# Kernel optimization log

Hardware: AMD Instinct MI355X
Metric: run time of the kernel (lower is better)

Reference implementation:

```python
import jax, jax.numpy as jnp
import numpy as np

BS, C_IN, CTX, TGT = 2, 8, 1024, 96
D_MODEL, N_HEADS, D_FF, N_LAYERS = 256, 16, 1024, 4
PF, SF, PC, SC = 8, 4, 32, 16
NF = (CTX + SF - PF) // SF + 1   # 256 fine patches (incl. end-pad)
NC = (CTX + SC - PC) // SC + 1   # 64 coarse patches
TOTAL = NF + NC                  # 320
EPS = 1e-5
DK = D_MODEL // N_HEADS
SCALE = DK ** -0.5


def _patchify(z, plen, stride):
    # ReplicationPad1d((0, stride)) then unfold -> (bs, c, n_patches, plen)
    pad = jnp.broadcast_to(z[..., -1:], z.shape[:-1] + (stride,))
    zp = jnp.concatenate([z, pad], axis=-1)
    n = (zp.shape[-1] - plen) // stride + 1
    idx = np.arange(n)[:, None] * stride + np.arange(plen)[None, :]
    return zp[..., idx]


def _layernorm(x, s, b):
    m = x.mean(-1, keepdims=True)
    v = jnp.var(x, axis=-1, keepdims=True)
    return (x - m) * jax.lax.rsqrt(v + EPS) * s + b


def setup_inputs() -> dict:
    key = jax.random.key(0)
    ks = jax.random.split(key, 16)
    g = lambda k, shape: jax.random.normal(k, shape, jnp.float32) * 0.02
    return {
        "z": jax.random.normal(ks[0], (BS, C_IN, CTX), jnp.float32),
        "revin_w": jnp.ones((C_IN,), jnp.float32),
        "revin_b": jnp.zeros((C_IN,), jnp.float32),
        "Wf": g(ks[1], (PF, D_MODEL)), "bf": jnp.zeros((D_MODEL,), jnp.float32),
        "Wc": g(ks[2], (PC, D_MODEL)), "bc": jnp.zeros((D_MODEL,), jnp.float32),
        "W_pos": jax.random.uniform(ks[3], (TOTAL, D_MODEL), jnp.float32, -0.02, 0.02),
        "WQ": g(ks[4], (N_LAYERS, D_MODEL, D_MODEL)), "bQ": jnp.zeros((N_LAYERS, D_MODEL), jnp.float32),
        "WK": g(ks[5], (N_LAYERS, D_MODEL, D_MODEL)), "bK": jnp.zeros((N_LAYERS, D_MODEL), jnp.float32),
        "WV": g(ks[6], (N_LAYERS, D_MODEL, D_MODEL)), "bV": jnp.zeros((N_LAYERS, D_MODEL), jnp.float32),
        "WO": g(ks[7], (N_LAYERS, D_MODEL, D_MODEL)), "bO": jnp.zeros((N_LAYERS, D_MODEL), jnp.float32),
        "ln1_s": jnp.ones((N_LAYERS, D_MODEL), jnp.float32), "ln1_b": jnp.zeros((N_LAYERS, D_MODEL), jnp.float32),
        "ln2_s": jnp.ones((N_LAYERS, D_MODEL), jnp.float32), "ln2_b": jnp.zeros((N_LAYERS, D_MODEL), jnp.float32),
        "F1": g(ks[8], (N_LAYERS, D_MODEL, D_FF)), "c1": jnp.zeros((N_LAYERS, D_FF), jnp.float32),
        "F2": g(ks[9], (N_LAYERS, D_FF, D_MODEL)), "c2": jnp.zeros((N_LAYERS, D_MODEL), jnp.float32),
        "Wh": g(ks[10], (D_MODEL * TOTAL, TGT)), "bh": jnp.zeros((TGT,), jnp.float32),
    }


def reference(z, revin_w, revin_b, Wf, bf, Wc, bc, W_pos, WQ, bQ, WK, bK, WV, bV,
              WO, bO, ln1_s, ln1_b, ln2_s, ln2_b, F1, c1, F2, c2, Wh, bh):
    # RevIN norm over the time axis (last axis of (bs, c, T))
    mean = z.mean(-1, keepdims=True)
    std = jnp.sqrt(jnp.var(z, axis=-1, keepdims=True) + EPS)
    zn = (z - mean) / std * revin_w[None, :, None] + revin_b[None, :, None]

    # dual-scale patch embedding
    x_fine = _patchify(zn, PF, SF) @ Wf + bf      # (bs, c, NF, d)
    x_coarse = _patchify(zn, PC, SC) @ Wc + bc    # (bs, c, NC, d)
    x = jnp.concatenate([x_fine, x_coarse], axis=2)  # (bs, c, TOTAL, d)

    u = x.reshape(BS * C_IN, TOTAL, D_MODEL) + W_pos  # (B, S, d), B=bs*c

    # residual-score transformer encoder (post-norm)
    prev = None
    for l in range(N_LAYERS):
        q = (u @ WQ[l] + bQ[l]).reshape(-1, TOTAL, N_HEADS, DK).transpose(0, 2, 1, 3)
        k = (u @ WK[l] + bK[l]).reshape(-1, TOTAL, N_HEADS, DK).transpose(0, 2, 1, 3)
        v = (u @ WV[l] + bV[l]).reshape(-1, TOTAL, N_HEADS, DK).transpose(0, 2, 1, 3)
        s = jnp.einsum('bhqd,bhkd->bhqk', q, k) * SCALE
        if prev is not None:
            s = s + prev
        w = jax.nn.softmax(s, axis=-1)
        o = jnp.einsum('bhqk,bhkd->bhqd', w, v).transpose(0, 2, 1, 3).reshape(-1, TOTAL, D_MODEL)
        o = o @ WO[l] + bO[l]
        u = _layernorm(u + o, ln1_s[l], ln1_b[l])
        h = jax.nn.gelu(u @ F1[l] + c1[l], approximate=False) @ F2[l] + c2[l]
        u = _layernorm(u + h, ln2_s[l], ln2_b[l])
        prev = s

    # head: (bs, c, TOTAL, d) -> permute -> flatten(d, TOTAL) -> linear
    zz = u.reshape(BS, C_IN, TOTAL, D_MODEL).transpose(0, 1, 3, 2).reshape(BS, C_IN, D_MODEL * TOTAL)
    out = zz @ Wh + bh  # (bs, c, TGT)

    # RevIN denorm
    out = (out - revin_b[None, :, None]) / (revin_w[None, :, None] + EPS * EPS) * std + mean
    return out
```

## Files before the change

kernel.cpp:

```cpp
#include <hip/hip_runtime.h>
#include <math.h>

typedef unsigned short ushort;
typedef unsigned int uint;
typedef __attribute__((ext_vector_type(8))) short short8;
typedef __attribute__((ext_vector_type(4))) float f32x4;
typedef __attribute__((ext_vector_type(4))) ushort us4;

constexpr int BS = 2, C_IN = 8, CTX = 1024, TGT = 96;
constexpr int DM = 256, NH = 16, DFF = 1024, NL = 4;
constexpr int NF = 256, TOTAL = 320;
constexpr int NB = 16;
constexpr int DK = 16;
constexpr float EPS = 1e-5f;
constexpr float SCALE = 0.25f;
constexpr int KHEAD = DM * TOTAL;

__device__ __forceinline__ ushort f2b(float x) {
    uint u = __float_as_uint(x);
    u += 0x7fff + ((u >> 16) & 1);
    return (ushort)(u >> 16);
}
__device__ __forceinline__ float bu2f(ushort x) { return __uint_as_float(((uint)x) << 16); }
__device__ __forceinline__ float lo2f(uint p) { return __uint_as_float(p << 16); }
__device__ __forceinline__ float hi2f(uint p) { return __uint_as_float(p & 0xffff0000u); }
__device__ __forceinline__ uint pack2(float a, float b) { return (uint)f2b(a) | ((uint)f2b(b) << 16); }

__global__ void k_convt(const float* __restrict__ src, ushort* __restrict__ dst,
                        int R, int C, int sls, int dls) {
    __shared__ ushort tile[32][33];
    src += (size_t)blockIdx.z * sls;
    dst += (size_t)blockIdx.z * dls;
    int c0 = blockIdx.x * 32, r0 = blockIdx.y * 32;
    int tx = threadIdx.x, ty = threadIdx.y;
    tile[ty][tx] = f2b(src[(r0 + ty) * C + c0 + tx]);
    __syncthreads();
    dst[(c0 + ty) * R + r0 + tx] = tile[tx][ty];
}

__global__ void k_revin(const float* __restrict__ z, const float* __restrict__ rw,
                        const float* __restrict__ rb, float* __restrict__ zn,
                        float* __restrict__ meanv, float* __restrict__ stdv) {
    int bc = blockIdx.x, t = threadIdx.x;
    __shared__ float r1[256], r2[256];
    float s1 = 0.f, s2 = 0.f;
    for (int i = t; i < CTX; i += 256) {
        float x = z[bc * CTX + i];
        s1 += x; s2 += x * x;
    }
    r1[t] = s1; r2[t] = s2; __syncthreads();
    for (int off = 128; off > 0; off >>= 1) {
        if (t < off) { r1[t] += r1[t + off]; r2[t] += r2[t + off]; }
        __syncthreads();
    }
    float m = r1[0] * (1.0f / CTX);
    float var = r2[0] * (1.0f / CTX) - m * m;
    float sd = sqrtf(var + EPS);
    float w = rw[bc % C_IN], b = rb[bc % C_IN];
    float inv = 1.0f / sd;
    for (int i = t; i < CTX; i += 256) {
        float x = z[bc * CTX + i];
        zn[bc * CTX + i] = (x - m) * inv * w + b;
    }
    if (t == 0) { meanv[bc] = m; stdv[bc] = sd; }
}

__global__ void k_embed(const float* __restrict__ zn, const float* __restrict__ Wf,
                        const float* __restrict__ bfv, const float* __restrict__ Wc,
                        const float* __restrict__ bcv, const float* __restrict__ Wpos,
                        ushort* __restrict__ u) {
    int bc = blockIdx.x / TOTAL, p = blockIdx.x % TOTAL, d = threadIdx.x;
    float acc;
    if (p < NF) {
        acc = bfv[d];
        int base = p * 4;
        for (int i = 0; i < 8; i++) {
            int idx = min(base + i, CTX - 1);
            acc += zn[bc * CTX + idx] * Wf[i * DM + d];
        }
    } else {
        int pc = p - NF;
        acc = bcv[d];
        int base = pc * 16;
        for (int i = 0; i < 32; i++) {
            int idx = min(base + i, CTX - 1);
            acc += zn[bc * CTX + idx] * Wc[i * DM + d];
        }
    }
    acc += Wpos[p * DM + d];
    u[(bc * TOTAL + p) * DM + d] = f2b(acc);
}

template <int GELU, int QKV>
__global__ __launch_bounds__(256) void k_gemm_mfma(const ushort* __restrict__ A,
                                                   const ushort* __restrict__ Wt,
                                                   const float* __restrict__ b0,
                                                   const float* __restrict__ b1,
                                                   const float* __restrict__ b2,
                                                   ushort* __restrict__ C,
                                                   int M, int N, int K) {
    __shared__ ushort As[64][40];
    __shared__ ushort Bs[64][40];
    int tid = threadIdx.x;
    int wave = tid >> 6, lane = tid & 63;
    int quad = lane >> 4, l16 = lane & 15;
    int m0 = blockIdx.y * 64, n0 = blockIdx.x * 64;

    f32x4 acc[4];
#pragma unroll
    for (int nt = 0; nt < 4; nt++) acc[nt] = (f32x4){0.f, 0.f, 0.f, 0.f};

    int row = tid >> 2, kc = (tid & 3) * 8;
    for (int k0 = 0; k0 < K; k0 += 32) {
        *(short8*)&As[row][kc] = *(const short8*)&A[(m0 + row) * K + k0 + kc];
        *(short8*)&Bs[row][kc] = *(const short8*)&Wt[(n0 + row) * K + k0 + kc];
        __syncthreads();
        short8 af = *(const short8*)&As[wave * 16 + l16][quad * 8];
#pragma unroll
        for (int nt = 0; nt < 4; nt++) {
            short8 bf = *(const short8*)&Bs[nt * 16 + l16][quad * 8];
            acc[nt] = __builtin_amdgcn_mfma_f32_16x16x32_bf16(af, bf, acc[nt], 0, 0, 0);
        }
        __syncthreads();
    }
#pragma unroll
    for (int nt = 0; nt < 4; nt++) {
        int col = n0 + nt * 16 + l16;
        float bi;
        if (QKV) {
            int bs = (n0 + nt * 16) >> 8;
            const float* bp = bs == 0 ? b0 : (bs == 1 ? b1 : b2);
            bi = bp[col & 255];
        } else {
            bi = b0[col];
        }
#pragma unroll
        for (int r = 0; r < 4; r++) {
            int rowm = m0 + wave * 16 + quad * 4 + r;
            float vv = acc[nt][r] + bi;
            if (GELU) vv = vv * 0.5f * (1.0f + erff(vv * 0.70710678118f));
            if (QKV) C[(col >> 8) * (M * DM) + rowm * DM + (col & 255)] = f2b(vv);
            else C[rowm * N + col] = f2b(vv);
        }
    }
}

__global__ __launch_bounds__(256, 4) void k_attn(const ushort* __restrict__ qm, const ushort* __restrict__ km,
                                                 const ushort* __restrict__ vm, uint4* __restrict__ sp,
                                                 ushort* __restrict__ ao, int mode) {
    __shared__ ushort sh[10240];
    uint* sh32 = (uint*)sh;
    int bh = blockIdx.x, b = bh >> 4, h = bh & 15;
    int i0 = blockIdx.y * 64;
    int t = threadIdx.x, wave = t >> 6, lane = t & 63, quad = lane >> 4, l16 = lane & 15;
    const short8 zero8 = (short8){0, 0, 0, 0, 0, 0, 0, 0};

    for (int idx = t; idx < 640; idx += 256) {
        int j = idx >> 1, half = idx & 1;
        short8 kv = *(const short8*)&km[(b * TOTAL + j) * DM + h * DK + half * 8];
        int jt = j >> 4, jl = j & 15;
        *(short8*)&sh[((jt * 2 + half) * 16 + jl) * 8] = kv;
    }
    for (int idx = t; idx < 320; idx += 256) {
        int jp = idx >> 1, dh = idx & 1;
        int j = jp * 2;
        uint4 a = *(const uint4*)&vm[(b * TOTAL + j) * DM + h * DK + dh * 8];
        uint4 bb = *(const uint4*)&vm[(b * TOTAL + j + 1) * DM + h * DK + dh * 8];
        const ushort* ap = (const ushort*)&a;
        const ushort* bp = (const ushort*)&bb;
        int jr = j & 31;
        int q = (jr & 15) >> 2, jj = ((jr >> 4) << 2) + (jr & 3);
        int base = 5120 + ((j >> 5) * 4 + q) * 128 + jj;
#pragma unroll
        for (int dd = 0; dd < 8; dd++) {
            int d = dh * 8 + dd;
            uint val = (uint)ap[dd] | ((uint)bp[dd] << 16);
            sh32[(base + d * 8) >> 1] = val;
        }
    }
    short8 qf = zero8;
    if (quad < 2) qf = *(const short8*)&qm[(b * TOTAL + i0 + wave * 16 + l16) * DM + h * DK + quad * 8];
    __syncthreads();

    f32x4 acc[20];
#pragma unroll
    for (int nt = 0; nt < 20; nt++) {
        short8 kf = *(const short8*)&sh[((nt * 2 + (quad & 1)) * 16 + l16) * 8];
        acc[nt] = __builtin_amdgcn_mfma_f32_16x16x32_bf16(kf, qf, (f32x4){0.f, 0.f, 0.f, 0.f}, 0, 0, 0);
    }

    int cb = (bh * 5 + (int)blockIdx.y) * 10 * 256 + t;
#pragma unroll
    for (int c = 0; c < 10; c++) {
        float e[8];
#pragma unroll
        for (int j = 0; j < 8; j++) e[j] = acc[2 * c + (j >> 2)][j & 3] * SCALE;
        if (mode) {
            uint4 pv = sp[cb + c * 256];
            e[0] += lo2f(pv.x); e[1] += hi2f(pv.x); e[2] += lo2f(pv.y); e[3] += hi2f(pv.y);
            e[4] += lo2f(pv.z); e[5] += hi2f(pv.z); e[6] += lo2f(pv.w); e[7] += hi2f(pv.w);
        }
        if (mode != 2) {
            uint4 ov;
            ov.x = pack2(e[0], e[1]); ov.y = pack2(e[2], e[3]);
            ov.z = pack2(e[4], e[5]); ov.w = pack2(e[6], e[7]);
            sp[cb + c * 256] = ov;
        }
#pragma unroll
        for (int j = 0; j < 8; j++) acc[2 * c + (j >> 2)][j & 3] = e[j];
    }

    float mx = -1e30f;
#pragma unroll
    for (int nt = 0; nt < 20; nt++)
#pragma unroll
        for (int r = 0; r < 4; r++) mx = fmaxf(mx, acc[nt][r]);
    mx = fmaxf(mx, __shfl_xor(mx, 16));
    mx = fmaxf(mx, __shfl_xor(mx, 32));
    float sum = 0.f;
#pragma unroll
    for (int nt = 0; nt < 20; nt++)
#pragma unroll
        for (int r = 0; r < 4; r++) { acc[nt][r] = __expf(acc[nt][r] - mx); sum += acc[nt][r]; }
    sum += __shfl_xor(sum, 16);
    sum += __shfl_xor(sum, 32);
    float inv = 1.f / sum;
#pragma unroll
    for (int nt = 0; nt < 20; nt++)
#pragma unroll
        for (int r = 0; r < 4; r++) acc[nt][r] *= inv;

    f32x4 oacc = (f32x4){0.f, 0.f, 0.f, 0.f};
#pragma unroll
    for (int jt2 = 0; jt2 < 10; jt2++) {
        short8 vt = *(const short8*)&sh[5120 + ((jt2 * 4 + quad) * 16 + l16) * 8];
        union { short8 v; uint u[4]; } pf;
        pf.u[0] = pack2(acc[2 * jt2][0], acc[2 * jt2][1]);
        pf.u[1] = pack2(acc[2 * jt2][2], acc[2 * jt2][3]);
        pf.u[2] = pack2(acc[2 * jt2 + 1][0], acc[2 * jt2 + 1][1]);
        pf.u[3] = pack2(acc[2 * jt2 + 1][2], acc[2 * jt2 + 1][3]);
        oacc = __builtin_amdgcn_mfma_f32_16x16x32_bf16(vt, pf.v, oacc, 0, 0, 0);
    }
    us4 ov4 = (us4){f2b(oacc[0]), f2b(oacc[1]), f2b(oacc[2]), f2b(oacc[3])};
    *(us4*)&ao[(b * TOTAL + i0 + wave * 16 + l16) * DM + h * DK + quad * 4] = ov4;
}

__global__ __launch_bounds__(256) void k_add_ln(ushort* __restrict__ u, const ushort* __restrict__ o,
                                                const float* __restrict__ ls, const float* __restrict__ lb) {
    int wave = threadIdx.x >> 6, lane = threadIdx.x & 63;
    int row = blockIdx.x * 4 + wave;
    int d0 = lane * 4;
    uint2 uv = *(const uint2*)&u[row * DM + d0];
    uint2 ov = *(const uint2*)&o[row * DM + d0];
    float x0 = lo2f(uv.x) + lo2f(ov.x);
    float x1 = hi2f(uv.x) + hi2f(ov.x);
    float x2 = lo2f(uv.y) + lo2f(ov.y);
    float x3 = hi2f(uv.y) + hi2f(ov.y);
    float sum = x0 + x1 + x2 + x3;
    float sq = x0 * x0 + x1 * x1 + x2 * x2 + x3 * x3;
#pragma unroll
    for (int off = 1; off < 64; off <<= 1) {
        sum += __shfl_xor(sum, off);
        sq += __shfl_xor(sq, off);
    }
    float m = sum * (1.0f / DM);
    float var = sq * (1.0f / DM) - m * m;
    float rs = rsqrtf(var + EPS);
    f32x4 sc = *(const f32x4*)&ls[d0];
    f32x4 bb = *(const f32x4*)&lb[d0];
    float y0 = (x0 - m) * rs * sc[0] + bb[0];
    float y1 = (x1 - m) * rs * sc[1] + bb[1];
    float y2 = (x2 - m) * rs * sc[2] + bb[2];
    float y3 = (x3 - m) * rs * sc[3] + bb[3];
    uint2 w;
    w.x = pack2(y0, y1); w.y = pack2(y2, y3);
    *(uint2*)&u[row * DM + d0] = w;
}

__global__ void k_transpose(const ushort* __restrict__ u, ushort* __restrict__ zzT) {
    __shared__ ushort tile[32][34];
    int bc = blockIdx.x, p0 = blockIdx.y * 32, d0 = blockIdx.z * 32;
    int tx = threadIdx.x, ty = threadIdx.y;
    tile[ty][tx] = u[(bc * TOTAL + p0 + ty) * DM + d0 + tx];
    __syncthreads();
    zzT[bc * (DM * TOTAL) + (d0 + ty) * TOTAL + p0 + tx] = tile[tx][ty];
}

__global__ __launch_bounds__(256) void k_head(const ushort* __restrict__ zzT, const ushort* __restrict__ WhT,
                                              float* __restrict__ acc_head) {
    int t0 = blockIdx.x * 16;
    int wave = threadIdx.x >> 6, lane = threadIdx.x & 63;
    int quad = lane >> 4, l16 = lane & 15;
    int kbeg = (blockIdx.y * 4 + wave) * 1024;
    f32x4 acc = (f32x4){0.f, 0.f, 0.f, 0.f};
    const ushort* za = &zzT[l16 * KHEAD + quad * 8];
    const ushort* wb = &WhT[(t0 + l16) * KHEAD + quad * 8];
#pragma unroll 4
    for (int k = kbeg; k < kbeg + 1024; k += 32) {
        short8 af = *(const short8*)&za[k];
        short8 bf = *(const short8*)&wb[k];
        acc = __builtin_amdgcn_mfma_f32_16x16x32_bf16(af, bf, acc, 0, 0, 0);
    }
#pragma unroll
    for (int r = 0; r < 4; r++)
        atomicAdd(&acc_head[(quad * 4 + r) * TGT + t0 + l16], acc[r]);
}

__global__ void k_final(const float* __restrict__ acc_head, const float* __restrict__ bh,
                        const float* __restrict__ rw, const float* __restrict__ rb,
                        const float* __restrict__ meanv, const float* __restrict__ stdv,
                        float* __restrict__ out) {
    int idx = blockIdx.x * 256 + threadIdx.x;
    if (idx >= NB * TGT) return;
    int bc = idx / TGT, t = idx % TGT, c = bc % C_IN;
    float vv = acc_head[idx] + bh[t];
    vv = (vv - rb[c]) / (rw[c] + EPS * EPS) * stdv[bc] + meanv[bc];
    out[idx] = vv;
}

extern "C" void kernel_launch(void* const* d_in, const int* in_sizes, int n_in,
                              void* d_out, int out_size, void* d_ws, size_t ws_size,
                              hipStream_t stream) {
    const float* z       = (const float*)d_in[0];
    const float* revin_w = (const float*)d_in[1];
    const float* revin_b = (const float*)d_in[2];
    const float* Wf      = (const float*)d_in[3];
    const float* bfv     = (const float*)d_in[4];
    const float* Wc      = (const float*)d_in[5];
    const float* bcv     = (const float*)d_in[6];
    const float* Wpos    = (const float*)d_in[7];
    const float* WQ      = (const float*)d_in[8];
    const float* bQ      = (const float*)d_in[9];
    const float* WK      = (const float*)d_in[10];
    const float* bK      = (const float*)d_in[11];
    const float* WV      = (const float*)d_in[12];
    const float* bV      = (const float*)d_in[13];
    const float* WO      = (const float*)d_in[14];
    const float* bO      = (const float*)d_in[15];
    const float* ln1s    = (const float*)d_in[16];
    const float* ln1b    = (const float*)d_in[17];
    const float* ln2s    = (const float*)d_in[18];
    const float* ln2b    = (const float*)d_in[19];
    const float* F1      = (const float*)d_in[20];
    const float* c1      = (const float*)d_in[21];
    const float* F2      = (const float*)d_in[22];
    const float* c2      = (const float*)d_in[23];
    const float* Wh      = (const float*)d_in[24];
    const float* bh      = (const float*)d_in[25];
    float* out = (float*)d_out;

    const int M = NB * TOTAL;

    char* p = (char*)d_ws;
    float* meanv = (float*)p;    p += 16 * 4;
    float* stdv  = (float*)p;    p += 16 * 4;
    float* acc_head = (float*)p; p += NB * TGT * 4;
    p = (char*)(((size_t)p + 255) & ~255ull);
    float* zn = (float*)p;       p += NB * CTX * 4;
    ushort* u    = (ushort*)p;   p += (size_t)M * DM * 2;
    ushort* qkv  = (ushort*)p;   p += (size_t)3 * M * DM * 2;
    ushort* ax   = (ushort*)p;   p += (size_t)M * DM * 2;
    ushort* o    = (ushort*)p;   p += (size_t)M * DM * 2;
    ushort* hbuf = (ushort*)p;   p += (size_t)M * DFF * 2;
    ushort* zzT  = (ushort*)p;   p += (size_t)M * DM * 2;
    ushort* Wtqkv = (ushort*)p;  p += (size_t)NL * 768 * 256 * 2;
    ushort* WtO   = (ushort*)p;  p += (size_t)NL * 256 * 256 * 2;
    ushort* Ft1   = (ushort*)p;  p += (size_t)NL * 1024 * 256 * 2;
    ushort* Ft2   = (ushort*)p;  p += (size_t)NL * 256 * 1024 * 2;
    ushort* WhT   = (ushort*)p;  p += (size_t)TGT * KHEAD * 2;
    p = (char*)(((size_t)p + 255) & ~255ull);
    uint4* sp = (uint4*)p;       p += (size_t)NB * NH * 5 * 10 * 256 * 16;

    k_convt<<<dim3(8, 8, 4), dim3(32, 32), 0, stream>>>(WQ, Wtqkv + 0,         256, 256, 65536, 768 * 256);
    k_convt<<<dim3(8, 8, 4), dim3(32, 32), 0, stream>>>(WK, Wtqkv + 256 * 256, 256, 256, 65536, 768 * 256);
    k_convt<<<dim3(8, 8, 4), dim3(32, 32), 0, stream>>>(WV, Wtqkv + 512 * 256, 256, 256, 65536, 768 * 256);
    k_convt<<<dim3(8, 8, 4), dim3(32, 32), 0, stream>>>(WO, WtO, 256, 256, 65536, 65536);
    k_convt<<<dim3(32, 8, 4), dim3(32, 32), 0, stream>>>(F1, Ft1, 256, 1024, 262144, 262144);
    k_convt<<<dim3(8, 32, 4), dim3(32, 32), 0, stream>>>(F2, Ft2, 1024, 256, 262144, 262144);
    k_convt<<<dim3(3, 2560, 1), dim3(32, 32), 0, stream>>>(Wh, WhT, KHEAD, TGT, 0, 0);

    k_revin<<<NB, 256, 0, stream>>>(z, revin_w, revin_b, zn, meanv, stdv);
    k_embed<<<NB * TOTAL, 256, 0, stream>>>(zn, Wf, bfv, Wc, bcv, Wpos, u);

    for (int l = 0; l < NL; l++) {
        int mode = (l == 0) ? 0 : (l == NL - 1 ? 2 : 1);
        k_gemm_mfma<0, 1><<<dim3(12, 80), 256, 0, stream>>>(
            u, Wtqkv + (size_t)l * 768 * 256, bQ + l * DM, bK + l * DM, bV + l * DM, qkv, M, 768, 256);
        k_attn<<<dim3(NB * NH, 5), 256, 0, stream>>>(qkv, qkv + M * DM, qkv + 2 * M * DM, sp, ax, mode);
        k_gemm_mfma<0, 0><<<dim3(4, 80), 256, 0, stream>>>(
            ax, WtO + (size_t)l * 65536, bO + l * DM, bO + l * DM, bO + l * DM, o, M, 256, 256);
        k_add_ln<<<M / 4, 256, 0, stream>>>(u, o, ln1s + l * DM, ln1b + l * DM);
        k_gemm_mfma<1, 0><<<dim3(16, 80), 256, 0, stream>>>(
            u, Ft1 + (size_t)l * 262144, c1 + l * DFF, c1, c1, hbuf, M, 1024, 256);
        k_gemm_mfma<0, 0><<<dim3(4, 80), 256, 0, stream>>>(
            hbuf, Ft2 + (size_t)l * 262144, c2 + l * DM, c2, c2, o, M, 256, 1024);
        k_add_ln<<<M / 4, 256, 0, stream>>>(u, o, ln2s + l * DM, ln2b + l * DM);
    }

    k_transpose<<<dim3(NB, TOTAL / 32, DM / 32), dim3(32, 32), 0, stream>>>(u, zzT);
    hipMemsetAsync(acc_head, 0, NB * TGT * sizeof(float), stream);
    k_head<<<dim3(TGT / 16, 20), 256, 0, stream>>>(zzT, WhT, acc_head);
    k_final<<<(NB * TGT + 255) / 256, 256, 0, stream>>>(acc_head, bh, revin_w, revin_b, meanv, stdv, out);
}
```

Before: 500.3 us.

## Fuse residual+LayerNorm into full-row GEMMs and drop final transpose

GEMM tiles are widened to 64x256 so each block owns full 256-wide output rows, which lets the residual add and LayerNorm run in the O-projection and FFN2 epilogues and removes the separate add_ln kernels and the intermediate o buffer. The head weight is re-permuted at conversion time so the head GEMM can read u directly, which removes the zzT transpose kernel. The four QKV/O weight conversions are merged into one launch. In exchange the LN GEMMs launch only 80 blocks with 64 accumulator registers per thread, so fewer blocks run in parallel.

After: 691.9 us. 1.38x slower.

```diff
diff --git a/kernel.cpp b/kernel.cpp
--- a/kernel.cpp
+++ b/kernel.cpp
@@ -15,6 +15,7 @@
 constexpr float EPS = 1e-5f;
 constexpr float SCALE = 0.25f;
 constexpr int KHEAD = DM * TOTAL;
+constexpr int M = NB * TOTAL;
 
 __device__ __forceinline__ ushort f2b(float x) {
     uint u = __float_as_uint(x);
@@ -36,6 +37,30 @@
     tile[ty][tx] = f2b(src[(r0 + ty) * C + c0 + tx]);
     __syncthreads();
     dst[(c0 + ty) * R + r0 + tx] = tile[tx][ty];
+}
+
+__global__ void k_convt_sq(const float* __restrict__ WQ, const float* __restrict__ WK,
+                           const float* __restrict__ WV, const float* __restrict__ WO,
+                           ushort* __restrict__ Wtqkv, ushort* __restrict__ WtO) {
+    __shared__ ushort tile[32][33];
+    int z = blockIdx.z, w = z >> 2, l = z & 3;
+    const float* src = (w == 0 ? WQ : (w == 1 ? WK : (w == 2 ? WV : WO))) + l * 65536;
+    ushort* dst = (w < 3) ? (Wtqkv + (size_t)l * 768 * 256 + w * 256 * 256)
+                          : (WtO + (size_t)l * 65536);
+    int c0 = blockIdx.x * 32, r0 = blockIdx.y * 32;
+    int tx = threadIdx.x, ty = threadIdx.y;
+    tile[ty][tx] = f2b(src[(r0 + ty) * 256 + c0 + tx]);
+    __syncthreads();
+    dst[(c0 + ty) * 256 + r0 + tx] = tile[tx][ty];
+}
+
+__global__ void k_convt_head(const float* __restrict__ Wh, ushort* __restrict__ WhT2) {
+    __shared__ ushort tile[32][33];
+    int t0 = blockIdx.x * 32, d0 = blockIdx.y * 32, p = blockIdx.z;
+    int tx = threadIdx.x, ty = threadIdx.y;
+    tile[ty][tx] = f2b(Wh[((size_t)(d0 + ty) * 320 + p) * 96 + t0 + tx]);
+    __syncthreads();
+    WhT2[(size_t)(t0 + ty) * KHEAD + p * 256 + d0 + tx] = tile[tx][ty];
 }
 
 __global__ void k_revin(const float* __restrict__ z, const float* __restrict__ rw,
@@ -91,56 +116,119 @@
     u[(bc * TOTAL + p) * DM + d] = f2b(acc);
 }
 
-template <int GELU, int QKV>
-__global__ __launch_bounds__(256) void k_gemm_mfma(const ushort* __restrict__ A,
-                                                   const ushort* __restrict__ Wt,
-                                                   const float* __restrict__ b0,
-                                                   const float* __restrict__ b1,
-                                                   const float* __restrict__ b2,
-                                                   ushort* __restrict__ C,
-                                                   int M, int N, int K) {
-    __shared__ ushort As[64][40];
-    __shared__ ushort Bs[64][40];
+__device__ __forceinline__ void gemm_core(const ushort* __restrict__ A, const ushort* __restrict__ Wt,
+                                          int K, int m0, ushort (*As)[40], ushort (*Bs)[40],
+                                          f32x4* acc) {
     int tid = threadIdx.x;
-    int wave = tid >> 6, lane = tid & 63;
-    int quad = lane >> 4, l16 = lane & 15;
-    int m0 = blockIdx.y * 64, n0 = blockIdx.x * 64;
-
-    f32x4 acc[4];
-#pragma unroll
-    for (int nt = 0; nt < 4; nt++) acc[nt] = (f32x4){0.f, 0.f, 0.f, 0.f};
-
+    int wave = tid >> 6, lane = tid & 63, quad = lane >> 4, l16 = lane & 15;
     int row = tid >> 2, kc = (tid & 3) * 8;
     for (int k0 = 0; k0 < K; k0 += 32) {
         *(short8*)&As[row][kc] = *(const short8*)&A[(m0 + row) * K + k0 + kc];
-        *(short8*)&Bs[row][kc] = *(const short8*)&Wt[(n0 + row) * K + k0 + kc];
+#pragma unroll
+        for (int i = 0; i < 4; i++)
+            *(short8*)&Bs[i * 64 + row][kc] = *(const short8*)&Wt[(i * 64 + row) * K + k0 + kc];
         __syncthreads();
         short8 af = *(const short8*)&As[wave * 16 + l16][quad * 8];
 #pragma unroll
-        for (int nt = 0; nt < 4; nt++) {
+        for (int nt = 0; nt < 16; nt++) {
             short8 bf = *(const short8*)&Bs[nt * 16 + l16][quad * 8];
             acc[nt] = __builtin_amdgcn_mfma_f32_16x16x32_bf16(af, bf, acc[nt], 0, 0, 0);
         }
         __syncthreads();
     }
-#pragma unroll
-    for (int nt = 0; nt < 4; nt++) {
-        int col = n0 + nt * 16 + l16;
-        float bi;
-        if (QKV) {
-            int bs = (n0 + nt * 16) >> 8;
-            const float* bp = bs == 0 ? b0 : (bs == 1 ? b1 : b2);
-            bi = bp[col & 255];
-        } else {
-            bi = b0[col];
-        }
+}
+
+__global__ __launch_bounds__(256, 2) void k_gemm_qkv(const ushort* __restrict__ u,
+                                                     const ushort* __restrict__ Wtl,
+                                                     const float* __restrict__ bQ,
+                                                     const float* __restrict__ bK,
+                                                     const float* __restrict__ bV,
+                                                     ushort* __restrict__ qkv) {
+    __shared__ ushort As[64][40];
+    __shared__ ushort Bs[256][40];
+    int m0 = blockIdx.x * 64, sl = blockIdx.y;
+    f32x4 acc[16];
+#pragma unroll
+    for (int nt = 0; nt < 16; nt++) acc[nt] = (f32x4){0.f, 0.f, 0.f, 0.f};
+    gemm_core(u, Wtl + sl * 256 * 256, 256, m0, As, Bs, acc);
+    int lane = threadIdx.x & 63, wave = threadIdx.x >> 6, quad = lane >> 4, l16 = lane & 15;
+    const float* bias = sl == 0 ? bQ : (sl == 1 ? bK : bV);
+    ushort* out = qkv + (size_t)sl * M * DM;
+#pragma unroll
+    for (int nt = 0; nt < 16; nt++) {
+        int col = nt * 16 + l16;
+        float bi = bias[col];
+#pragma unroll
+        for (int r = 0; r < 4; r++) {
+            int rowm = m0 + wave * 16 + quad * 4 + r;
+            out[rowm * DM + col] = f2b(acc[nt][r] + bi);
+        }
+    }
+}
+
+__global__ __launch_bounds__(256, 2) void k_gemm_gelu(const ushort* __restrict__ u,
+                                                      const ushort* __restrict__ Wtl,
+                                                      const float* __restrict__ bias,
+                                                      ushort* __restrict__ hbuf) {
+    __shared__ ushort As[64][40];
+    __shared__ ushort Bs[256][40];
+    int m0 = blockIdx.x * 64, n0 = blockIdx.y * 256;
+    f32x4 acc[16];
+#pragma unroll
+    for (int nt = 0; nt < 16; nt++) acc[nt] = (f32x4){0.f, 0.f, 0.f, 0.f};
+    gemm_core(u, Wtl + (size_t)n0 * 256, 256, m0, As, Bs, acc);
+    int lane = threadIdx.x & 63, wave = threadIdx.x >> 6, quad = lane >> 4, l16 = lane & 15;
+#pragma unroll
+    for (int nt = 0; nt < 16; nt++) {
+        int col = nt * 16 + l16;
+        float bi = bias[n0 + col];
 #pragma unroll
         for (int r = 0; r < 4; r++) {
             int rowm = m0 + wave * 16 + quad * 4 + r;
             float vv = acc[nt][r] + bi;
-            if (GELU) vv = vv * 0.5f * (1.0f + erff(vv * 0.70710678118f));
-            if (QKV) C[(col >> 8) * (M * DM) + rowm * DM + (col & 255)] = f2b(vv);
-            else C[rowm * N + col] = f2b(vv);
+            vv = vv * 0.5f * (1.0f + erff(vv * 0.70710678118f));
+            hbuf[rowm * DFF + n0 + col] = f2b(vv);
+        }
+    }
+}
+
+__global__ __launch_bounds__(256, 2) void k_gemm_ln(const ushort* __restrict__ A,
+                                                    const ushort* __restrict__ Wtl,
+                                                    const float* __restrict__ bias,
+                                                    const float* __restrict__ ls,
+                                                    const float* __restrict__ lb,
+                                                    ushort* __restrict__ u, int K) {
+    __shared__ ushort As[64][40];
+    __shared__ ushort Bs[256][40];
+    int m0 = blockIdx.x * 64;
+    f32x4 acc[16];
+#pragma unroll
+    for (int nt = 0; nt < 16; nt++) acc[nt] = (f32x4){0.f, 0.f, 0.f, 0.f};
+    gemm_core(A, Wtl, K, m0, As, Bs, acc);
+    int lane = threadIdx.x & 63, wave = threadIdx.x >> 6, quad = lane >> 4, l16 = lane & 15;
+#pragma unroll
+    for (int r = 0; r < 4; r++) {
+        int rowm = m0 + wave * 16 + quad * 4 + r;
+        ushort* up = &u[rowm * DM];
+        float xv[16];
+        float s1 = 0.f, s2 = 0.f;
+#pragma unroll
+        for (int nt = 0; nt < 16; nt++) {
+            int col = nt * 16 + l16;
+            float x = acc[nt][r] + bias[col] + bu2f(up[col]);
+            xv[nt] = x; s1 += x; s2 += x * x;
+        }
+        s1 += __shfl_xor(s1, 1); s2 += __shfl_xor(s2, 1);
+        s1 += __shfl_xor(s1, 2); s2 += __shfl_xor(s2, 2);
+        s1 += __shfl_xor(s1, 4); s2 += __shfl_xor(s2, 4);
+        s1 += __shfl_xor(s1, 8); s2 += __shfl_xor(s2, 8);
+        float m = s1 * (1.0f / DM);
+        float var = s2 * (1.0f / DM) - m * m;
+        float rs = rsqrtf(var + EPS);
+#pragma unroll
+        for (int nt = 0; nt < 16; nt++) {
+            int col = nt * 16 + l16;
+            up[col] = f2b((xv[nt] - m) * rs * ls[col] + lb[col]);
         }
     }
 }
@@ -245,56 +333,15 @@
     *(us4*)&ao[(b * TOTAL + i0 + wave * 16 + l16) * DM + h * DK + quad * 4] = ov4;
 }
 
-__global__ __launch_bounds__(256) void k_add_ln(ushort* __restrict__ u, const ushort* __restrict__ o,
-                                                const float* __restrict__ ls, const float* __restrict__ lb) {
-    int wave = threadIdx.x >> 6, lane = threadIdx.x & 63;
-    int row = blockIdx.x * 4 + wave;
-    int d0 = lane * 4;
-    uint2 uv = *(const uint2*)&u[row * DM + d0];
-    uint2 ov = *(const uint2*)&o[row * DM + d0];
-    float x0 = lo2f(uv.x) + lo2f(ov.x);
-    float x1 = hi2f(uv.x) + hi2f(ov.x);
-    float x2 = lo2f(uv.y) + lo2f(ov.y);
-    float x3 = hi2f(uv.y) + hi2f(ov.y);
-    float sum = x0 + x1 + x2 + x3;
-    float sq = x0 * x0 + x1 * x1 + x2 * x2 + x3 * x3;
-#pragma unroll
-    for (int off = 1; off < 64; off <<= 1) {
-        sum += __shfl_xor(sum, off);
-        sq += __shfl_xor(sq, off);
-    }
-    float m = sum * (1.0f / DM);
-    float var = sq * (1.0f / DM) - m * m;
-    float rs = rsqrtf(var + EPS);
-    f32x4 sc = *(const f32x4*)&ls[d0];
-    f32x4 bb = *(const f32x4*)&lb[d0];
-    float y0 = (x0 - m) * rs * sc[0] + bb[0];
-    float y1 = (x1 - m) * rs * sc[1] + bb[1];
-    float y2 = (x2 - m) * rs * sc[2] + bb[2];
-    float y3 = (x3 - m) * rs * sc[3] + bb[3];
-    uint2 w;
-    w.x = pack2(y0, y1); w.y = pack2(y2, y3);
-    *(uint2*)&u[row * DM + d0] = w;
-}
-
-__global__ void k_transpose(const ushort* __restrict__ u, ushort* __restrict__ zzT) {
-    __shared__ ushort tile[32][34];
-    int bc = blockIdx.x, p0 = blockIdx.y * 32, d0 = blockIdx.z * 32;
-    int tx = threadIdx.x, ty = threadIdx.y;
-    tile[ty][tx] = u[(bc * TOTAL + p0 + ty) * DM + d0 + tx];
-    __syncthreads();
-    zzT[bc * (DM * TOTAL) + (d0 + ty) * TOTAL + p0 + tx] = tile[tx][ty];
-}
-
-__global__ __launch_bounds__(256) void k_head(const ushort* __restrict__ zzT, const ushort* __restrict__ WhT,
+__global__ __launch_bounds__(256) void k_head(const ushort* __restrict__ u, const ushort* __restrict__ WhT2,
                                               float* __restrict__ acc_head) {
     int t0 = blockIdx.x * 16;
     int wave = threadIdx.x >> 6, lane = threadIdx.x & 63;
     int quad = lane >> 4, l16 = lane & 15;
     int kbeg = (blockIdx.y * 4 + wave) * 1024;
     f32x4 acc = (f32x4){0.f, 0.f, 0.f, 0.f};
-    const ushort* za = &zzT[l16 * KHEAD + quad * 8];
-    const ushort* wb = &WhT[(t0 + l16) * KHEAD + quad * 8];
+    const ushort* za = &u[(size_t)l16 * KHEAD + quad * 8];
+    const ushort* wb = &WhT2[(size_t)(t0 + l16) * KHEAD + quad * 8];
 #pragma unroll 4
     for (int k = kbeg; k < kbeg + 1024; k += 32) {
         short8 af = *(const short8*)&za[k];
@@ -349,8 +396,6 @@
     const float* bh      = (const float*)d_in[25];
     float* out = (float*)d_out;
 
-    const int M = NB * TOTAL;
-
     char* p = (char*)d_ws;
     float* meanv = (float*)p;    p += 16 * 4;
     float* stdv  = (float*)p;    p += 16 * 4;
@@ -360,45 +405,37 @@
     ushort* u    = (ushort*)p;   p += (size_t)M * DM * 2;
     ushort* qkv  = (ushort*)p;   p += (size_t)3 * M * DM * 2;
     ushort* ax   = (ushort*)p;   p += (size_t)M * DM * 2;
-    ushort* o    = (ushort*)p;   p += (size_t)M * DM * 2;
     ushort* hbuf = (ushort*)p;   p += (size_t)M * DFF * 2;
-    ushort* zzT  = (ushort*)p;   p += (size_t)M * DM * 2;
     ushort* Wtqkv = (ushort*)p;  p += (size_t)NL * 768 * 256 * 2;
     ushort* WtO   = (ushort*)p;  p += (size_t)NL * 256 * 256 * 2;
     ushort* Ft1   = (ushort*)p;  p += (size_t)NL * 1024 * 256 * 2;
     ushort* Ft2   = (ushort*)p;  p += (size_t)NL * 256 * 1024 * 2;
-    ushort* WhT   = (ushort*)p;  p += (size_t)TGT * KHEAD * 2;
+    ushort* WhT2  = (ushort*)p;  p += (size_t)TGT * KHEAD * 2;
     p = (char*)(((size_t)p + 255) & ~255ull);
     uint4* sp = (uint4*)p;       p += (size_t)NB * NH * 5 * 10 * 256 * 16;
 
-    k_convt<<<dim3(8, 8, 4), dim3(32, 32), 0, stream>>>(WQ, Wtqkv + 0,         256, 256, 65536, 768 * 256);
-    k_convt<<<dim3(8, 8, 4), dim3(32, 32), 0, stream>>>(WK, Wtqkv + 256 * 256, 256, 256, 65536, 768 * 256);
-    k_convt<<<dim3(8, 8, 4), dim3(32, 32), 0, stream>>>(WV, Wtqkv + 512 * 256, 256, 256, 65536, 768 * 256);
-    k_convt<<<dim3(8, 8, 4), dim3(32, 32), 0, stream>>>(WO, WtO, 256, 256, 65536, 65536);
+    k_convt_sq<<<dim3(8, 8, 16), dim3(32, 32), 0, stream>>>(WQ, WK, WV, WO, Wtqkv, WtO);
     k_convt<<<dim3(32, 8, 4), dim3(32, 32), 0, stream>>>(F1, Ft1, 256, 1024, 262144, 262144);
     k_convt<<<dim3(8, 32, 4), dim3(32, 32), 0, stream>>>(F2, Ft2, 1024, 256, 262144, 262144);
-    k_convt<<<dim3(3, 2560, 1), dim3(32, 32), 0, stream>>>(Wh, WhT, KHEAD, TGT, 0, 0);
+    k_convt_head<<<dim3(3, 8, 320), dim3(32, 32), 0, stream>>>(Wh, WhT2);
 
     k_revin<<<NB, 256, 0, stream>>>(z, revin_w, revin_b, zn, meanv, stdv);
     k_embed<<<NB * TOTAL, 256, 0, stream>>>(zn, Wf, bfv, Wc, bcv, Wpos, u);
 
     for (int l = 0; l < NL; l++) {
         int mode = (l == 0) ? 0 : (l == NL - 1 ? 2 : 1);
-        k_gemm_mfma<0, 1><<<dim3(12, 80), 256, 0, stream>>>(
-            u, Wtqkv + (size_t)l * 768 * 256, bQ + l * DM, bK + l * DM, bV + l * DM, qkv, M, 768, 256);
+        k_gemm_qkv<<<dim3(M / 64, 3), 256, 0, stream>>>(
+            u, Wtqkv + (size_t)l * 768 * 256, bQ + l * DM, bK + l * DM, bV + l * DM, qkv);
         k_attn<<<dim3(NB * NH, 5), 256, 0, stream>>>(qkv, qkv + M * DM, qkv + 2 * M * DM, sp, ax, mode);
-        k_gemm_mfma<0, 0><<<dim3(4, 80), 256, 0, stream>>>(
-            ax, WtO + (size_t)l * 65536, bO + l * DM, bO + l * DM, bO + l * DM, o, M, 256, 256);
-        k_add_ln<<<M / 4, 256, 0, stream>>>(u, o, ln1s + l * DM, ln1b + l * DM);
-        k_gemm_mfma<1, 0><<<dim3(16, 80), 256, 0, stream>>>(
-            u, Ft1 + (size_t)l * 262144, c1 + l * DFF, c1, c1, hbuf, M, 1024, 256);
-        k_gemm_mfma<0, 0><<<dim3(4, 80), 256, 0, stream>>>(
-            hbuf, Ft2 + (size_t)l * 262144, c2 + l * DM, c2, c2, o, M, 256, 1024);
-        k_add_ln<<<M / 4, 256, 0, stream>>>(u, o, ln2s + l * DM, ln2b + l * DM);
-    }
-
-    k_transpose<<<dim3(NB, TOTAL / 32, DM / 32), dim3(32, 32), 0, stream>>>(u, zzT);
+        k_gemm_ln<<<M / 64, 256, 0, stream>>>(
+            ax, WtO + (size_t)l * 65536, bO + l * DM, ln1s + l * DM, ln1b + l * DM, u, 256);
+        k_gemm_gelu<<<dim3(M / 64, 4), 256, 0, stream>>>(
+            u, Ft1 + (size_t)l * 262144, c1 + l * DFF, hbuf);
+        k_gemm_ln<<<M / 64, 256, 0, stream>>>(
+            hbuf, Ft2 + (size_t)l * 262144, c2 + l * DM, ln2s + l * DM, ln2b + l * DM, u, 1024);
+    }
+
     hipMemsetAsync(acc_head, 0, NB * TGT * sizeof(float), stream);
-    k_head<<<dim3(TGT / 16, 20), 256, 0, stream>>>(zzT, WhT, acc_head);
+    k_head<<<dim3(TGT / 16, 20), 256, 0, stream>>>(u, WhT2, acc_head);
     k_final<<<(NB * TGT + 255) / 256, 256, 0, stream>>>(acc_head, bh, revin_w, revin_b, meanv, stdv, out);
 }
```
